# Optimization experiments

Measured on AMD Instinct MI355X. Metric: run time of the kernel, lower is better.

The kernel has to match this reference:

```python
import jax, jax.numpy as jnp
import numpy as np

START_IDX = 1  # Offsets.GO
END_IDX = 2    # Offsets.EOS
NEG_INF = -10000.0


def setup_inputs() -> dict:
    key = jax.random.key(0)
    k1, k2, k3 = jax.random.split(key, 3)
    B, T, N = 256, 1024, 128
    unary = jax.random.normal(k1, (B, T, N), dtype=jnp.float32)
    trans = jax.random.normal(k2, (1, N, N), dtype=jnp.float32) * 0.1
    lengths = jax.random.randint(k3, (B,), 1, T + 1)
    return {"unary": unary, "trans": trans, "lengths": lengths}


def _forward_alg(unary_btn, trans, lengths):
    """CRF log-partition. unary_btn: [B,T,N], trans: [1,N,N], lengths: [B] -> [B]."""
    B, T, N = unary_btn.shape
    tr = trans[0]  # [N(cur), N(prev)]
    unary_tbn = jnp.transpose(unary_btn, (1, 0, 2))  # batch_first -> [T,B,N]

    init_alphas = jnp.full((B, N), NEG_INF, dtype=unary_btn.dtype)
    init_alphas = init_alphas.at[:, START_IDX].set(0.0)

    def step(alphas, inp):
        unary_t, t = inp  # unary_t: [B,N]
        # scores[b, i, j] = alphas[b, j] + trans[i, j] + unary_t[b, i]
        scores = alphas[:, None, :] + tr[None, :, :] + unary_t[:, :, None]
        new_alphas = jax.nn.logsumexp(scores, axis=2)  # [B,N]
        # only advance positions still inside the sequence
        alphas = jnp.where((t < lengths)[:, None], new_alphas, alphas)
        return alphas, None

    alphas, _ = jax.lax.scan(step, init_alphas, (unary_tbn, jnp.arange(T)))
    terminal = alphas + tr[END_IDX][None, :]  # trans[:, end_idx] row: [N]
    return jax.nn.logsumexp(terminal, axis=1)  # [B]


def reference(unary, trans, lengths):
    return _forward_alg(unary, trans, lengths)
```

## Files before the change

### kernel.cpp

```cpp
#include <hip/hip_runtime.h>

#define T_LEN 1024
#define NS    128
#define BT    16
#define G     16
#define SEG   32
#define SSH   5
#define NB    256

typedef __attribute__((ext_vector_type(8))) short short8;
typedef __attribute__((ext_vector_type(4))) short short4v;
typedef __attribute__((ext_vector_type(4))) float f32x4;

static __device__ __forceinline__ short f2bf(float f) {
    unsigned u = __builtin_bit_cast(unsigned, f);
    u = (u + 0x7fffu + ((u >> 16) & 1u)) >> 16;
    return (short)u;
}
static __device__ __forceinline__ float bf2f(short s) {
    unsigned u = ((unsigned)(unsigned short)s) << 16;
    return __builtin_bit_cast(float, u);
}
static __device__ __forceinline__ short f2bf_trunc(float f) {
    return (short)(__builtin_bit_cast(unsigned, f) >> 16);
}

__global__ __launch_bounds__(64, 1) void crf_seg(
        const float* __restrict__ unary, const float* __restrict__ trans,
        const int* __restrict__ lengths,
        float* __restrict__ yv, float* __restrict__ zv,
        float* __restrict__ cfv, float* __restrict__ cbv) {
    __shared__ __align__(16) short Fs[BT * NS];

    const int tid = threadIdx.x;
    const int g = blockIdx.x & (G - 1);
    const int u = blockIdx.x >> 4;
    const bool bwd = u >= (SEG - 1);
    const int s = bwd ? (u - (SEG - 2)) : u;
    const int quad = tid >> 4, bcol = tid & 15;

    const int Lb = lengths[g * BT + bcol];
    const int tb = (s * Lb) >> SSH, te = ((s + 1) * Lb) >> SSH;
    const int nrec = te - tb - 1;
    int dlen = te - tb;
    #pragma unroll
    for (int m = 1; m < 16; m <<= 1) {
        int o = __shfl_xor(dlen, m, 64);
        dlen = o > dlen ? o : dlen;
    }
    const int iters = dlen;

    short8 Ea[8][4];
    #pragma unroll
    for (int j = 0; j < 8; ++j) {
        const int i = j * 16 + bcol;
        #pragma unroll
        for (int kt = 0; kt < 4; ++kt) {
            short8 e;
            if (!bwd) {
                const float* tr = trans + (size_t)i * NS + kt * 32 + quad * 8;
                float4 x = *(const float4*)tr, y = *(const float4*)(tr + 4);
                e[0] = f2bf(__expf(x.x)); e[1] = f2bf(__expf(x.y));
                e[2] = f2bf(__expf(x.z)); e[3] = f2bf(__expf(x.w));
                e[4] = f2bf(__expf(y.x)); e[5] = f2bf(__expf(y.y));
                e[6] = f2bf(__expf(y.z)); e[7] = f2bf(__expf(y.w));
            } else {
                #pragma unroll
                for (int jj = 0; jj < 8; ++jj)
                    e[jj] = f2bf(__expf(trans[(size_t)(kt * 32 + quad * 8 + jj) * NS + i]));
            }
            Ea[j][kt] = e;
        }
    }

    #pragma unroll
    for (int rep = 0; rep < 4; ++rep) {
        const int tv = rep * 64 + tid;
        const int sr = tv >> 4, sc = tv & 15;
        const int Ls = lengths[g * BT + sr];
        const int s_tb = (s * Ls) >> SSH, s_te = ((s + 1) * Ls) >> SSH;
        const float* ubase = unary + (size_t)(g * BT + sr) * T_LEN * NS + sc * 8;
        float v[8];
        if (!bwd) {
            #pragma unroll
            for (int k = 0; k < 8; ++k)
                v[k] = (s == 0) ? ((sc * 8 + k == 1) ? 1.f : 0.f) : 1.f;
        } else {
            int ti = s_te - 1; if (ti < 0) ti = 0;
            const float* up = ubase + (size_t)ti * NS;
            float4 ua = *(const float4*)up, ub4 = *(const float4*)(up + 4);
            float uu[8] = {ua.x, ua.y, ua.z, ua.w, ub4.x, ub4.y, ub4.z, ub4.w};
            #pragma unroll
            for (int k = 0; k < 8; ++k) {
                float vv = (s == SEG - 1) ? __expf(trans[2 * NS + sc * 8 + k]) : 1.f;
                v[k] = __expf(uu[k]) * vv;
            }
        }
        short8 z;
        #pragma unroll
        for (int k = 0; k < 8; ++k) z[k] = f2bf(v[k]);
        *(short8*)&Fs[sr * NS + ((sc ^ sr) << 3)] = z;

        if (s_te == s_tb) {
            if (!bwd) {
                float* yp = yv + ((size_t)s * NB + g * BT + sr) * NS + sc * 8;
                #pragma unroll
                for (int k = 0; k < 8; ++k)
                    yp[k] = (s == 0) ? ((sc * 8 + k == 1) ? 1.f : 0.f) : 1.f;
                if (sc == 0) cfv[s * NB + g * BT + sr] = 0.f;
            } else {
                float* zp = zv + ((size_t)(s - 1) * NB + g * BT + sr) * NS + sc * 8;
                #pragma unroll
                for (int k = 0; k < 8; ++k) zp[k] = 1.f;
                if (sc == 0) cbv[(s - 1) * NB + g * BT + sr] = 0.f;
            }
        }
    }

    const float* uptr = unary + (size_t)(g * BT + bcol) * T_LEN * NS + quad * 4;
    #define T_OFB(nn) ({ int _t = bwd ? (te - 2 - (nn)) : (tb + (nn)); \
                         _t = _t < 0 ? 0 : (_t > T_LEN - 1 ? T_LEN - 1 : _t); _t; })
    float4 pA[8], pB[8];
    {
        int t = T_OFB(0);
        #pragma unroll
        for (int j = 0; j < 8; ++j) pA[j] = *(const float4*)(uptr + (size_t)t * NS + j * 16);
        t = T_OFB(1);
        #pragma unroll
        for (int j = 0; j < 8; ++j) pB[j] = *(const float4*)(uptr + (size_t)t * NS + j * 16);
    }

    int bfOff[4];
    #pragma unroll
    for (int kt = 0; kt < 4; ++kt) bfOff[kt] = bcol * NS + (((kt * 4 + quad) ^ bcol) << 3);
    const int s4Off = bcol * NS + (bcol << 3);
    int fwo[8];
    #pragma unroll
    for (int j = 0; j < 8; ++j) {
        const int cj = 2 * j + (quad >> 1);
        fwo[j] = bcol * NS + ((cj ^ bcol) << 3) + ((quad & 1) << 2);
    }

    asm volatile("s_waitcnt lgkmcnt(0)" ::: "memory");
    float C = 0.f;

#define STEP(U) do {                                                              \
    short8 Bf0 = *(const short8*)&Fs[bfOff[0]];                                   \
    short8 Bf1 = *(const short8*)&Fs[bfOff[1]];                                   \
    short8 Bf2 = *(const short8*)&Fs[bfOff[2]];                                   \
    short8 Bf3 = *(const short8*)&Fs[bfOff[3]];                                   \
    short4v s4 = *(const short4v*)&Fs[s4Off];                                     \
    float e_[8][4];                                                               \
    _Pragma("unroll")                                                             \
    for (int j = 0; j < 8; ++j) {                                                 \
        e_[j][0] = __expf(U[j].x); e_[j][1] = __expf(U[j].y);                     \
        e_[j][2] = __expf(U[j].z); e_[j][3] = __expf(U[j].w);                     \
    }                                                                             \
    { int t = T_OFB(n + 2);                                                       \
      _Pragma("unroll")                                                           \
      for (int j = 0; j < 8; ++j)                                                 \
          U[j] = *(const float4*)(uptr + (size_t)t * NS + j * 16); }              \
    f32x4 acc[8];                                                                 \
    _Pragma("unroll")                                                             \
    for (int j = 0; j < 8; ++j) acc[j] = (f32x4){0.f, 0.f, 0.f, 0.f};             \
    _Pragma("unroll")                                                             \
    for (int j = 0; j < 8; ++j) acc[j] = __builtin_amdgcn_mfma_f32_16x16x32_bf16(Ea[j][0], Bf0, acc[j], 0, 0, 0); \
    _Pragma("unroll")                                                             \
    for (int j = 0; j < 8; ++j) acc[j] = __builtin_amdgcn_mfma_f32_16x16x32_bf16(Ea[j][1], Bf1, acc[j], 0, 0, 0); \
    _Pragma("unroll")                                                             \
    for (int j = 0; j < 8; ++j) acc[j] = __builtin_amdgcn_mfma_f32_16x16x32_bf16(Ea[j][2], Bf2, acc[j], 0, 0, 0); \
    _Pragma("unroll")                                                             \
    for (int j = 0; j < 8; ++j) acc[j] = __builtin_amdgcn_mfma_f32_16x16x32_bf16(Ea[j][3], Bf3, acc[j], 0, 0, 0); \
    float sv = (bf2f(s4[0]) + bf2f(s4[1])) + (bf2f(s4[2]) + bf2f(s4[3]));         \
    float rs = __fdividef(1.f, sv);                                               \
    float logs = __logf(sv);                                                      \
    float fn[8][4];                                                               \
    _Pragma("unroll")                                                             \
    for (int j = 0; j < 8; ++j) {                                                 \
        fn[j][0] = acc[j][0] * e_[j][0] * rs; fn[j][1] = acc[j][1] * e_[j][1] * rs; \
        fn[j][2] = acc[j][2] * e_[j][2] * rs; fn[j][3] = acc[j][3] * e_[j][3] * rs; \
    }                                                                             \
    if (n == nrec) {                                                              \
        if (!bwd) {              \
            float* yp = yv + ((size_t)s * NB + g * BT + bcol) * NS;               \
            _Pragma("unroll")                                                     \
            for (int j = 0; j < 8; ++j)                                           \
                *(float4*)(yp + j * 16 + quad * 4) = (float4){fn[j][0], fn[j][1], fn[j][2], fn[j][3]}; \
            if (tid < BT) cfv[s * NB + g * BT + tid] = C + logs;                  \
        } else {                  \
            float* zp = zv + ((size_t)(s - 1) * NB + g * BT + bcol) * NS;         \
            _Pragma("unroll")                                                     \
            for (int j = 0; j < 8; ++j)                                           \
                *(float4*)(zp + j * 16 + quad * 4) = (float4){acc[j][0], acc[j][1], acc[j][2], acc[j][3]}; \
            if (tid < BT) cbv[(s - 1) * NB + g * BT + tid] = C;                   \
        }                                                                         \
    }                                                                             \
    C += logs;                                                                    \
    _Pragma("unroll")                                                             \
    for (int j = 0; j < 8; ++j) {                                                 \
        short4v p;                                                                \
        p[0] = f2bf_trunc(fn[j][0]); p[1] = f2bf_trunc(fn[j][1]);                 \
        p[2] = f2bf_trunc(fn[j][2]); p[3] = f2bf_trunc(fn[j][3]);                 \
        *(short4v*)&Fs[fwo[j]] = p;                                               \
    }                                                                             \
                      \
    asm volatile("s_waitcnt lgkmcnt(0)" ::: "memory");                            \
} while (0)

    for (int n = 0; n < iters; ) {
        STEP(pA); ++n;
        if (n >= iters) break;
        STEP(pB); ++n;
    }
#undef STEP
#undef T_OFB
}

__global__ __launch_bounds__(64) void crf_combine(
        const float* __restrict__ yv, const float* __restrict__ zv,
        const float* __restrict__ cfv, const float* __restrict__ cbv,
        float* __restrict__ out) {
    const int b = blockIdx.x, lane = threadIdx.x;
    float acc = cfv[b];
    for (int s = 1; s <= SEG - 1; ++s) acc += cbv[(s - 1) * NB + b];
    float lg = 0.f;
    for (int s = 1; s <= SEG - 1; ++s) {
        const float* Z = zv + ((size_t)(s - 1) * NB + b) * NS;
        const float* Y = yv + ((size_t)(s - 1) * NB + b) * NS;
        float d = Z[lane] * Y[lane] + Z[lane + 64] * Y[lane + 64];
        #pragma unroll
        for (int off = 1; off < 64; off <<= 1) d += __shfl_xor(d, off, 64);
        lg += __logf(d);
    }
    for (int s = 1; s <= SEG - 2; ++s) {
        const float* Y = yv + ((size_t)s * NB + b) * NS;
        float t = Y[lane] + Y[lane + 64];
        #pragma unroll
        for (int off = 1; off < 64; off <<= 1) t += __shfl_xor(t, off, 64);
        lg -= __logf(t);
    }
    if (lane == 0) out[b] = acc + lg;
}

extern "C" void kernel_launch(void* const* d_in, const int* in_sizes, int n_in,
                              void* d_out, int out_size, void* d_ws, size_t ws_size,
                              hipStream_t stream) {
    const float* unary   = (const float*)d_in[0];
    const float* trans   = (const float*)d_in[1];
    const int*   lengths = (const int*)d_in[2];
    float* out = (float*)d_out;

    float* yv  = (float*)d_ws;
    float* zv  = yv + (size_t)(SEG - 1) * NB * NS;
    float* cfv = zv + (size_t)(SEG - 1) * NB * NS;
    float* cbv = cfv + (size_t)(SEG - 1) * NB;

    crf_seg<<<dim3(2 * (SEG - 1) * G), dim3(64), 0, stream>>>(
        unary, trans, lengths, yv, zv, cfv, cbv);
    crf_combine<<<dim3(NB), dim3(64), 0, stream>>>(yv, zv, cfv, cbv, out);
}
```

Measured before the change: 250.4 us.

## Double sequence segments, single-buffer unary prefetch, parallelize combine across four waves

Raises the number of time segments from 32 to 64. This halves the serial recurrence length per block and doubles the grid, with launch bounds now allowing two waves per SIMD. The step loop is restructured from a two-buffer macro to a single prefetch buffer. The exp/scale is fused into the accumulators and the next timestep's load is issued after the MFMAs. The combine kernel splits the per-segment reductions across four waves with a shared-memory final sum. This adds more segment boundary work and bf16 approximation in exchange for shorter sequential chains.

After: 245.6 us. No clear change (-1.9%).

```diff
diff --git a/kernel.cpp b/kernel.cpp
--- a/kernel.cpp
+++ b/kernel.cpp
@@ -4,8 +4,8 @@
 #define NS    128
 #define BT    16
 #define G     16
-#define SEG   32
-#define SSH   5
+#define SEG   64
+#define SSH   6
 #define NB    256
 
 typedef __attribute__((ext_vector_type(8))) short short8;
@@ -25,7 +25,7 @@
     return (short)(__builtin_bit_cast(unsigned, f) >> 16);
 }
 
-__global__ __launch_bounds__(64, 1) void crf_seg(
+__global__ __launch_bounds__(64, 2) void crf_seg(
         const float* __restrict__ unary, const float* __restrict__ trans,
         const int* __restrict__ lengths,
         float* __restrict__ yv, float* __restrict__ zv,
@@ -120,14 +120,11 @@
     const float* uptr = unary + (size_t)(g * BT + bcol) * T_LEN * NS + quad * 4;
     #define T_OFB(nn) ({ int _t = bwd ? (te - 2 - (nn)) : (tb + (nn)); \
                          _t = _t < 0 ? 0 : (_t > T_LEN - 1 ? T_LEN - 1 : _t); _t; })
-    float4 pA[8], pB[8];
+    float4 U[8];
     {
         int t = T_OFB(0);
         #pragma unroll
-        for (int j = 0; j < 8; ++j) pA[j] = *(const float4*)(uptr + (size_t)t * NS + j * 16);
-        t = T_OFB(1);
-        #pragma unroll
-        for (int j = 0; j < 8; ++j) pB[j] = *(const float4*)(uptr + (size_t)t * NS + j * 16);
+        for (int j = 0; j < 8; ++j) U[j] = *(const float4*)(uptr + (size_t)t * NS + j * 16);
     }
 
     int bfOff[4];
@@ -144,87 +141,80 @@
     asm volatile("s_waitcnt lgkmcnt(0)" ::: "memory");
     float C = 0.f;
 
-#define STEP(U) do {                                                              \
-    short8 Bf0 = *(const short8*)&Fs[bfOff[0]];                                   \
-    short8 Bf1 = *(const short8*)&Fs[bfOff[1]];                                   \
-    short8 Bf2 = *(const short8*)&Fs[bfOff[2]];                                   \
-    short8 Bf3 = *(const short8*)&Fs[bfOff[3]];                                   \
-    short4v s4 = *(const short4v*)&Fs[s4Off];                                     \
-    float e_[8][4];                                                               \
-    _Pragma("unroll")                                                             \
-    for (int j = 0; j < 8; ++j) {                                                 \
-        e_[j][0] = __expf(U[j].x); e_[j][1] = __expf(U[j].y);                     \
-        e_[j][2] = __expf(U[j].z); e_[j][3] = __expf(U[j].w);                     \
-    }                                                                             \
-    { int t = T_OFB(n + 2);                                                       \
-      _Pragma("unroll")                                                           \
-      for (int j = 0; j < 8; ++j)                                                 \
-          U[j] = *(const float4*)(uptr + (size_t)t * NS + j * 16); }              \
-    f32x4 acc[8];                                                                 \
-    _Pragma("unroll")                                                             \
-    for (int j = 0; j < 8; ++j) acc[j] = (f32x4){0.f, 0.f, 0.f, 0.f};             \
-    _Pragma("unroll")                                                             \
-    for (int j = 0; j < 8; ++j) acc[j] = __builtin_amdgcn_mfma_f32_16x16x32_bf16(Ea[j][0], Bf0, acc[j], 0, 0, 0); \
-    _Pragma("unroll")                                                             \
-    for (int j = 0; j < 8; ++j) acc[j] = __builtin_amdgcn_mfma_f32_16x16x32_bf16(Ea[j][1], Bf1, acc[j], 0, 0, 0); \
-    _Pragma("unroll")                                                             \
-    for (int j = 0; j < 8; ++j) acc[j] = __builtin_amdgcn_mfma_f32_16x16x32_bf16(Ea[j][2], Bf2, acc[j], 0, 0, 0); \
-    _Pragma("unroll")                                                             \
-    for (int j = 0; j < 8; ++j) acc[j] = __builtin_amdgcn_mfma_f32_16x16x32_bf16(Ea[j][3], Bf3, acc[j], 0, 0, 0); \
-    float sv = (bf2f(s4[0]) + bf2f(s4[1])) + (bf2f(s4[2]) + bf2f(s4[3]));         \
-    float rs = __fdividef(1.f, sv);                                               \
-    float logs = __logf(sv);                                                      \
-    float fn[8][4];                                                               \
-    _Pragma("unroll")                                                             \
-    for (int j = 0; j < 8; ++j) {                                                 \
-        fn[j][0] = acc[j][0] * e_[j][0] * rs; fn[j][1] = acc[j][1] * e_[j][1] * rs; \
-        fn[j][2] = acc[j][2] * e_[j][2] * rs; fn[j][3] = acc[j][3] * e_[j][3] * rs; \
-    }                                                                             \
-    if (n == nrec) {                                                              \
-        if (!bwd) {              \
-            float* yp = yv + ((size_t)s * NB + g * BT + bcol) * NS;               \
-            _Pragma("unroll")                                                     \
-            for (int j = 0; j < 8; ++j)                                           \
-                *(float4*)(yp + j * 16 + quad * 4) = (float4){fn[j][0], fn[j][1], fn[j][2], fn[j][3]}; \
-            if (tid < BT) cfv[s * NB + g * BT + tid] = C + logs;                  \
-        } else {                  \
-            float* zp = zv + ((size_t)(s - 1) * NB + g * BT + bcol) * NS;         \
-            _Pragma("unroll")                                                     \
-            for (int j = 0; j < 8; ++j)                                           \
-                *(float4*)(zp + j * 16 + quad * 4) = (float4){acc[j][0], acc[j][1], acc[j][2], acc[j][3]}; \
-            if (tid < BT) cbv[(s - 1) * NB + g * BT + tid] = C;                   \
-        }                                                                         \
-    }                                                                             \
-    C += logs;                                                                    \
-    _Pragma("unroll")                                                             \
-    for (int j = 0; j < 8; ++j) {                                                 \
-        short4v p;                                                                \
-        p[0] = f2bf_trunc(fn[j][0]); p[1] = f2bf_trunc(fn[j][1]);                 \
-        p[2] = f2bf_trunc(fn[j][2]); p[3] = f2bf_trunc(fn[j][3]);                 \
-        *(short4v*)&Fs[fwo[j]] = p;                                               \
-    }                                                                             \
-                      \
-    asm volatile("s_waitcnt lgkmcnt(0)" ::: "memory");                            \
-} while (0)
-
-    for (int n = 0; n < iters; ) {
-        STEP(pA); ++n;
-        if (n >= iters) break;
-        STEP(pB); ++n;
-    }
-#undef STEP
+    for (int n = 0; n < iters; ++n) {
+        short8 Bf0 = *(const short8*)&Fs[bfOff[0]];
+        short8 Bf1 = *(const short8*)&Fs[bfOff[1]];
+        short8 Bf2 = *(const short8*)&Fs[bfOff[2]];
+        short8 Bf3 = *(const short8*)&Fs[bfOff[3]];
+        short4v s4 = *(const short4v*)&Fs[s4Off];
+
+        float sv = (bf2f(s4[0]) + bf2f(s4[1])) + (bf2f(s4[2]) + bf2f(s4[3]));
+        float rs = __fdividef(1.f, sv);
+        float logs = __logf(sv);
+
+        f32x4 acc[8];
+        #pragma unroll
+        for (int j = 0; j < 8; ++j) acc[j] = (f32x4){0.f, 0.f, 0.f, 0.f};
+        #pragma unroll
+        for (int j = 0; j < 8; ++j) acc[j] = __builtin_amdgcn_mfma_f32_16x16x32_bf16(Ea[j][0], Bf0, acc[j], 0, 0, 0);
+        #pragma unroll
+        for (int j = 0; j < 8; ++j) acc[j] = __builtin_amdgcn_mfma_f32_16x16x32_bf16(Ea[j][1], Bf1, acc[j], 0, 0, 0);
+        #pragma unroll
+        for (int j = 0; j < 8; ++j) acc[j] = __builtin_amdgcn_mfma_f32_16x16x32_bf16(Ea[j][2], Bf2, acc[j], 0, 0, 0);
+        #pragma unroll
+        for (int j = 0; j < 8; ++j) acc[j] = __builtin_amdgcn_mfma_f32_16x16x32_bf16(Ea[j][3], Bf3, acc[j], 0, 0, 0);
+
+        if (bwd && n == nrec) {
+            float* zp = zv + ((size_t)(s - 1) * NB + g * BT + bcol) * NS;
+            #pragma unroll
+            for (int j = 0; j < 8; ++j)
+                *(float4*)(zp + j * 16 + quad * 4) = (float4){acc[j][0], acc[j][1], acc[j][2], acc[j][3]};
+            if (tid < BT) cbv[(s - 1) * NB + g * BT + tid] = C;
+        }
+
+        {
+            int t = T_OFB(n + 1);
+            #pragma unroll
+            for (int j = 0; j < 8; ++j) {
+                float e0 = __expf(U[j].x), e1 = __expf(U[j].y);
+                float e2 = __expf(U[j].z), e3 = __expf(U[j].w);
+                acc[j][0] *= e0 * rs; acc[j][1] *= e1 * rs;
+                acc[j][2] *= e2 * rs; acc[j][3] *= e3 * rs;
+                U[j] = *(const float4*)(uptr + (size_t)t * NS + j * 16);
+            }
+        }
+
+        if (!bwd && n == nrec) {
+            float* yp = yv + ((size_t)s * NB + g * BT + bcol) * NS;
+            #pragma unroll
+            for (int j = 0; j < 8; ++j)
+                *(float4*)(yp + j * 16 + quad * 4) = (float4){acc[j][0], acc[j][1], acc[j][2], acc[j][3]};
+            if (tid < BT) cfv[s * NB + g * BT + tid] = C + logs;
+        }
+        C += logs;
+
+        #pragma unroll
+        for (int j = 0; j < 8; ++j) {
+            short4v p;
+            p[0] = f2bf_trunc(acc[j][0]); p[1] = f2bf_trunc(acc[j][1]);
+            p[2] = f2bf_trunc(acc[j][2]); p[3] = f2bf_trunc(acc[j][3]);
+            *(short4v*)&Fs[fwo[j]] = p;
+        }
+        asm volatile("s_waitcnt lgkmcnt(0)" ::: "memory");
+    }
 #undef T_OFB
 }
 
-__global__ __launch_bounds__(64) void crf_combine(
+__global__ __launch_bounds__(256) void crf_combine(
         const float* __restrict__ yv, const float* __restrict__ zv,
         const float* __restrict__ cfv, const float* __restrict__ cbv,
         float* __restrict__ out) {
-    const int b = blockIdx.x, lane = threadIdx.x;
-    float acc = cfv[b];
-    for (int s = 1; s <= SEG - 1; ++s) acc += cbv[(s - 1) * NB + b];
+    __shared__ float part[4];
+    const int b = blockIdx.x, tid = threadIdx.x;
+    const int w = tid >> 6, lane = tid & 63;
     float lg = 0.f;
-    for (int s = 1; s <= SEG - 1; ++s) {
+    for (int s = 1 + w; s <= SEG - 1; s += 4) lg += cbv[(s - 1) * NB + b];
+    for (int s = 1 + w; s <= SEG - 1; s += 4) {
         const float* Z = zv + ((size_t)(s - 1) * NB + b) * NS;
         const float* Y = yv + ((size_t)(s - 1) * NB + b) * NS;
         float d = Z[lane] * Y[lane] + Z[lane + 64] * Y[lane + 64];
@@ -232,14 +222,16 @@
         for (int off = 1; off < 64; off <<= 1) d += __shfl_xor(d, off, 64);
         lg += __logf(d);
     }
-    for (int s = 1; s <= SEG - 2; ++s) {
+    for (int s = 1 + w; s <= SEG - 2; s += 4) {
         const float* Y = yv + ((size_t)s * NB + b) * NS;
         float t = Y[lane] + Y[lane + 64];
         #pragma unroll
         for (int off = 1; off < 64; off <<= 1) t += __shfl_xor(t, off, 64);
         lg -= __logf(t);
     }
-    if (lane == 0) out[b] = acc + lg;
+    if (lane == 0) part[w] = lg;
+    __syncthreads();
+    if (tid == 0) out[b] = cfv[b] + ((part[0] + part[1]) + (part[2] + part[3]));
 }
 
 extern "C" void kernel_launch(void* const* d_in, const int* in_sizes, int n_in,
@@ -257,5 +249,5 @@
 
     crf_seg<<<dim3(2 * (SEG - 1) * G), dim3(64), 0, stream>>>(
         unary, trans, lengths, yv, zv, cfv, cbv);
-    crf_combine<<<dim3(NB), dim3(64), 0, stream>>>(yv, zv, cfv, cbv, out);
-}
+    crf_combine<<<dim3(NB), dim3(256), 0, stream>>>(yv, zv, cfv, cbv, out);
+}
```
